# Kernel tuning notes

Measured on AMD Instinct MI355X. Metric: run time of the kernel, lower is better.

## Reference

```python
import jax, jax.numpy as jnp
import numpy as np

SEQ = 4096
EMB = 1024
OUT = 1024


def setup_inputs() -> dict:
    key = jax.random.key(0)
    k_x, k_q, k_k, k_v = jax.random.split(key, 4)
    scale = 1.0 / np.sqrt(EMB)
    inputs = jax.random.normal(k_x, (SEQ, EMB), dtype=jnp.float32)
    # torch Linear weight is (out_features, in_features); y = x @ W.T
    W_Q = jax.random.normal(k_q, (OUT, EMB), dtype=jnp.float32) * scale
    W_K = jax.random.normal(k_k, (OUT, EMB), dtype=jnp.float32) * scale
    W_V = jax.random.normal(k_v, (OUT, EMB), dtype=jnp.float32) * scale
    return {"inputs": inputs, "W_Q": W_Q, "W_K": W_K, "W_V": W_V}


def reference(inputs, W_Q, W_K, W_V):
    # projections: (S, E) @ (E, D) -> (S, D)
    q = inputs @ W_Q.T
    k = inputs @ W_K.T
    v = inputs @ W_V.T
    d_k = k.shape[-1]
    scores = (q @ k.T) / jnp.sqrt(jnp.asarray(d_k, dtype=q.dtype))  # (S, S)
    weights = jax.nn.softmax(scores, axis=-1)
    return weights @ v  # (S, D)
```

## Files before the change

kernel.cpp:

```cpp
#include <hip/hip_runtime.h>

typedef __bf16 bf16;
typedef __bf16 bf16x4 __attribute__((ext_vector_type(4)));
typedef __bf16 bf16x8 __attribute__((ext_vector_type(8)));
typedef float f32x4 __attribute__((ext_vector_type(4)));

#define SEQ 4096
#define EMB 1024

__device__ __forceinline__ void async_copy16(void* lds, const void* g) {
    __builtin_amdgcn_global_load_lds(
        (const __attribute__((address_space(1))) unsigned int*)g,
        (__attribute__((address_space(3))) unsigned int*)lds,
        16, 0, 0);
}

__global__ __launch_bounds__(256) void prep_all(const float* __restrict__ x,
                                                const float* __restrict__ wq,
                                                const float* __restrict__ wk,
                                                const float* __restrict__ wv,
                                                bf16* __restrict__ xb,
                                                bf16* __restrict__ wqk,
                                                bf16* __restrict__ wvb,
                                                float* __restrict__ rowsum)
{
    const int u = blockIdx.x * 256 + threadIdx.x;
    const float* src;
    bf16* dst;
    int off;
    if (u < 1048576)      { src = x;  dst = xb;               off = u; }
    else if (u < 1310720) { src = wq; dst = wqk;              off = u - 1048576; }
    else if (u < 1572864) { src = wk; dst = wqk + EMB * EMB;  off = u - 1310720; }
    else if (u < 1835008) { src = wv; dst = wvb;              off = u - 1572864; }
    else {
        *(float4*)(rowsum + (size_t)(u - 1835008) * 4) = float4{0.f, 0.f, 0.f, 0.f};
        return;
    }
    float4 f = *(const float4*)(src + (size_t)off * 4);
    bf16x4 v = { (bf16)f.x, (bf16)f.y, (bf16)f.z, (bf16)f.w };
    *(bf16x4*)(dst + (size_t)off * 4) = v;
}

template<bool RSUM>
__device__ __forceinline__ void tile_step(int t, int NT,
                                          const bf16* __restrict__ Ab,
                                          const bf16* __restrict__ Bb,
                                          int lda, int ldb,
                                          bf16* __restrict__ As,
                                          bf16* __restrict__ Bs,
                                          bf16* __restrict__ AsD,
                                          bf16* __restrict__ BsD,
                                          int wr, int wc, int fr, int pc,
                                          bf16x8 (&afA)[4], bf16x8 (&afB)[4],
                                          bf16x8 (&bgC)[4], bf16x8 (&bgN)[4],
                                          f32x4 (&acc)[8][4], float (&rsum)[8],
                                          bool rs_active)
{
    if (t + 3 < NT) {
        const int b3 = ((t + 3) & 3) * 8192;
        async_copy16(AsD + b3,        Ab + (t + 3) * 32);
        async_copy16(AsD + b3 + 4096, Ab + (t + 3) * 32 + (size_t)128 * lda);
    }
    {
        const bf16* At = As + (t & 3) * 8192 + (wr * 128 + 64 + fr) * 32 + pc;
#pragma unroll
        for (int mf = 0; mf < 4; mf++)
            afB[mf] = *(const bf16x8*)(At + (mf * 16) * 32);
    }
    asm volatile("s_waitcnt lgkmcnt(4)" ::: "memory");
    __builtin_amdgcn_sched_barrier(0);
    __builtin_amdgcn_s_setprio(1);
#pragma unroll
    for (int nj = 0; nj < 4; nj++)
#pragma unroll
        for (int mf = 0; mf < 4; mf++)
            acc[mf][nj] = __builtin_amdgcn_mfma_f32_16x16x32_bf16(afA[mf], bgC[nj], acc[mf][nj], 0, 0, 0);
    __builtin_amdgcn_s_setprio(0);
    if (RSUM && rs_active) {
#pragma unroll
        for (int mf = 0; mf < 4; mf++)
#pragma unroll
            for (int e = 0; e < 8; e++) rsum[mf] += (float)afA[mf][e];
    }

    if (t < NT - 1) {
        if (t + 3 < NT) {
            asm volatile("s_waitcnt vmcnt(6)" ::: "memory");
        } else if (t + 2 < NT) {
            asm volatile("s_waitcnt vmcnt(4)" ::: "memory");
        } else {
            asm volatile("s_waitcnt vmcnt(0)" ::: "memory");
        }
        __builtin_amdgcn_s_barrier();
        if (t + 3 < NT) {
            const int b3 = ((t + 3) & 3) * 8192;
            async_copy16(BsD + b3,        Bb + (t + 3) * 32);
            async_copy16(BsD + b3 + 4096, Bb + (t + 3) * 32 + (size_t)128 * ldb);
        }
        {
            const int b1 = ((t + 1) & 3) * 8192;
            const bf16* At = As + b1 + (wr * 128 + fr) * 32 + pc;
            const bf16* Bt = Bs + b1 + (wc * 64 + fr) * 32 + pc;
#pragma unroll
            for (int mf = 0; mf < 4; mf++)
                afA[mf] = *(const bf16x8*)(At + (mf * 16) * 32);
#pragma unroll
            for (int nj = 0; nj < 4; nj++)
                bgN[nj] = *(const bf16x8*)(Bt + (nj * 16) * 32);
        }
        asm volatile("s_waitcnt lgkmcnt(8)" ::: "memory");
        __builtin_amdgcn_sched_barrier(0);
    } else {
        asm volatile("s_waitcnt lgkmcnt(0)" ::: "memory");
        __builtin_amdgcn_sched_barrier(0);
    }
    __builtin_amdgcn_s_setprio(1);
#pragma unroll
    for (int nj = 0; nj < 4; nj++)
#pragma unroll
        for (int mf = 0; mf < 4; mf++)
            acc[4 + mf][nj] = __builtin_amdgcn_mfma_f32_16x16x32_bf16(afB[mf], bgC[nj], acc[4 + mf][nj], 0, 0, 0);
    __builtin_amdgcn_s_setprio(0);
    if (RSUM && rs_active) {
#pragma unroll
        for (int mf = 0; mf < 4; mf++)
#pragma unroll
            for (int e = 0; e < 8; e++) rsum[4 + mf] += (float)afB[mf][e];
    }
}

template<bool RSUM>
__device__ __forceinline__ void gemm_core256(const bf16* __restrict__ A,
                                             const bf16* __restrict__ B,
                                             int lda, int ldb, long koff,
                                             int m0, int n0,
                                             bf16* __restrict__ As,
                                             bf16* __restrict__ Bs,
                                             f32x4 (&acc)[8][4], float (&rsum)[8],
                                             bool rs_active)
{
    const int tid  = threadIdx.x;
    const int lane = tid & 63;
    const int wave = tid >> 6;
    const int wr = wave >> 2;
    const int wc = wave & 3;
    const int srow = tid >> 2;
    const int spc  = tid & 3;
    const int sl   = (spc - ((srow >> 1) & 3)) & 3;
    const int fr = lane & 15;
    const int q  = lane >> 4;
    const int pc = ((q + ((fr >> 1) & 3)) & 3) * 8;
    const int NT = 32;

#pragma unroll
    for (int i = 0; i < 8; i++)
#pragma unroll
        for (int j = 0; j < 4; j++) acc[i][j] = {0.f, 0.f, 0.f, 0.f};
    if (RSUM)
#pragma unroll
        for (int i = 0; i < 8; i++) rsum[i] = 0.f;

    const bf16* Ab = A + (size_t)(m0 + srow) * lda + koff + sl * 8;
    const bf16* Bb = B + (size_t)(n0 + srow) * ldb + koff + sl * 8;
    bf16* AsD = As + srow * 32 + spc * 8;
    bf16* BsD = Bs + srow * 32 + spc * 8;

#pragma unroll
    for (int tt = 0; tt < 3; tt++) {
        async_copy16(AsD + tt * 8192,        Ab + tt * 32);
        async_copy16(AsD + tt * 8192 + 4096, Ab + tt * 32 + (size_t)128 * lda);
        async_copy16(BsD + tt * 8192,        Bb + tt * 32);
        async_copy16(BsD + tt * 8192 + 4096, Bb + tt * 32 + (size_t)128 * ldb);
    }
    asm volatile("s_waitcnt vmcnt(8)" ::: "memory");
    __builtin_amdgcn_s_barrier();

    bf16x8 afA[4], afB[4], bg0[4], bg1[4];
    {
        const bf16* At = As + (wr * 128 + fr) * 32 + pc;
        const bf16* Bt = Bs + (wc * 64 + fr) * 32 + pc;
#pragma unroll
        for (int mf = 0; mf < 4; mf++)
            afA[mf] = *(const bf16x8*)(At + (mf * 16) * 32);
#pragma unroll
        for (int nj = 0; nj < 4; nj++)
            bg0[nj] = *(const bf16x8*)(Bt + (nj * 16) * 32);
    }

    for (int t = 0; t < NT; t += 2) {
        tile_step<RSUM>(t,     NT, Ab, Bb, lda, ldb, As, Bs, AsD, BsD,
                        wr, wc, fr, pc, afA, afB, bg0, bg1, acc, rsum, rs_active);
        tile_step<RSUM>(t + 1, NT, Ab, Bb, lda, ldb, As, Bs, AsD, BsD,
                        wr, wc, fr, pc, afA, afB, bg1, bg0, acc, rsum, rs_active);
    }
}

__global__ __launch_bounds__(512, 1) void gemm_proj(const bf16* __restrict__ xb,
                                                    const bf16* __restrict__ wqk,
                                                    const bf16* __restrict__ wvb,
                                                    bf16* __restrict__ QK,
                                                    bf16* __restrict__ VT)
{
    __shared__ __align__(16) bf16 As[4][8192];
    __shared__ __align__(16) bf16 Bs[4][8192];

    const int hw  = blockIdx.x + 16 * blockIdx.y;
    const int xcd = hw & 7;
    const int s   = hw >> 3;
    const int bx  = ((xcd & 1) << 3) | (s & 7);
    const int byy = (xcd >> 1) * 3 + (s >> 3);

    const bf16 *A, *B;
    bf16* C;
    int ldc, m0, n0;
    if (byy < 8) {
        A = xb; B = wqk; C = QK; ldc = 2048;
        m0 = bx * 256; n0 = byy * 256;
    } else {
        const int id = bx + (byy - 8) * 16;
        A = wvb; B = xb; C = VT; ldc = 4096;
        m0 = (id & 3) * 256; n0 = (id >> 2) * 256;
    }

    f32x4 acc[8][4];
    float rs[8];
    gemm_core256<false>(A, B, 1024, 1024, 0, m0, n0, &As[0][0], &Bs[0][0], acc, rs, false);

    const int lane = threadIdx.x & 63;
    const int wave = threadIdx.x >> 6;
    const int cm = m0 + (wave >> 2) * 128 + ((lane >> 4) << 2);
    const int cn = n0 + (wave & 3) * 64 + (lane & 15);
#pragma unroll
    for (int i = 0; i < 8; i++)
#pragma unroll
        for (int j = 0; j < 4; j++)
#pragma unroll
            for (int r = 0; r < 4; r++)
                C[(size_t)(cm + i * 16 + r) * ldc + (cn + j * 16)] = (bf16)acc[i][j][r];
}

__global__ __launch_bounds__(512, 1) void gemm_exp(const bf16* __restrict__ QK,
                                                   bf16* __restrict__ E)
{
    __shared__ __align__(16) bf16 As[4][8192];
    __shared__ __align__(16) bf16 Bs[4][8192];

    const int hw  = blockIdx.x + 16 * blockIdx.y;
    const int xcd = hw & 7;
    const int s   = hw >> 3;
    const int bx  = ((xcd & 1) << 3) | (s & 7);
    const int by  = ((xcd >> 1) << 2) | (s >> 3);

    const int m0 = bx * 256;
    const int n0 = by * 256;
    f32x4 acc[8][4];
    float rs[8];
    gemm_core256<false>(QK, QK + 1024, 2048, 2048, 0, m0, n0, &As[0][0], &Bs[0][0], acc, rs, false);

    const int lane = threadIdx.x & 63;
    const int wave = threadIdx.x >> 6;
    const int cm = m0 + (wave >> 2) * 128 + ((lane >> 4) << 2);
    const int cn = n0 + (wave & 3) * 64 + (lane & 15);
#pragma unroll
    for (int i = 0; i < 8; i++)
#pragma unroll
        for (int j = 0; j < 4; j++)
#pragma unroll
            for (int r = 0; r < 4; r++)
                E[(size_t)(cm + i * 16 + r) * 4096 + (cn + j * 16)] =
                    (bf16)__expf(acc[i][j][r] * 0.03125f);
}

__global__ __launch_bounds__(512, 1) void gemm_pv(const bf16* __restrict__ E,
                                                  const bf16* __restrict__ VT,
                                                  float* __restrict__ out,
                                                  float* __restrict__ p1,
                                                  float* __restrict__ rowsum)
{
    __shared__ __align__(16) bf16 As[4][8192];
    __shared__ __align__(16) bf16 Bs[4][8192];

    const int hw  = blockIdx.x + 16 * blockIdx.y + 64 * blockIdx.z;
    const int xcd = hw & 7;
    const int s   = hw >> 3;
    const int bx  = ((xcd & 1) << 3) | (s & 7);
    const int by  = s >> 3;
    const int bz  = xcd >> 1;

    const int m0 = bx * 256;
    const int n0 = by * 256;
    const long koff = (long)bz * 1024;
    const bool rs_active = (by == 0) && (((threadIdx.x >> 6) & 3) == 0);

    f32x4 acc[8][4];
    float rs[8];
    gemm_core256<true>(E, VT, 4096, 4096, koff, m0, n0, &As[0][0], &Bs[0][0], acc, rs, rs_active);

    const int lane = threadIdx.x & 63;
    const int wave = threadIdx.x >> 6;
    if (rs_active) {
#pragma unroll
        for (int i = 0; i < 8; i++) {
            rs[i] += __shfl_xor(rs[i], 16);
            rs[i] += __shfl_xor(rs[i], 32);
        }
        if (lane < 16) {
            const int rbase = m0 + (wave >> 2) * 128;
#pragma unroll
            for (int i = 0; i < 8; i++)
                unsafeAtomicAdd(&rowsum[rbase + i * 16 + lane], rs[i]);
        }
    }

    float* C = (bz == 0) ? out : p1 + (size_t)(bz - 1) * SEQ * 1024;
    const int cm = m0 + (wave >> 2) * 128 + ((lane >> 4) << 2);
    const int cn = n0 + (wave & 3) * 64 + (lane & 15);
#pragma unroll
    for (int i = 0; i < 8; i++)
#pragma unroll
        for (int j = 0; j < 4; j++)
#pragma unroll
            for (int r = 0; r < 4; r++)
                C[(size_t)(cm + i * 16 + r) * 1024 + (cn + j * 16)] = acc[i][j][r];
}

__global__ __launch_bounds__(256) void reduce_norm(float* __restrict__ out,
                                                   const float* __restrict__ p1,
                                                   const float* __restrict__ p2,
                                                   const float* __restrict__ p3,
                                                   const float* __restrict__ rowsum)
{
    const int m = blockIdx.x;
    const float inv = 1.f / rowsum[m];
    const size_t off = (size_t)m * 1024 + threadIdx.x * 4;
    float4 a = *(const float4*)(out + off);
    float4 b = *(const float4*)(p1 + off);
    float4 c = *(const float4*)(p2 + off);
    float4 d = *(const float4*)(p3 + off);
    float4 o;
    o.x = (a.x + b.x + c.x + d.x) * inv;
    o.y = (a.y + b.y + c.y + d.y) * inv;
    o.z = (a.z + b.z + c.z + d.z) * inv;
    o.w = (a.w + b.w + c.w + d.w) * inv;
    *(float4*)(out + off) = o;
}

extern "C" void kernel_launch(void* const* d_in, const int* in_sizes, int n_in,
                              void* d_out, int out_size, void* d_ws, size_t ws_size,
                              hipStream_t stream)
{
    const float* x  = (const float*)d_in[0];
    const float* wq = (const float*)d_in[1];
    const float* wk = (const float*)d_in[2];
    const float* wv = (const float*)d_in[3];
    float* out = (float*)d_out;

    char* ws = (char*)d_ws;
    const size_t MB = 1024 * 1024;
    bf16*  E   = (bf16*)(ws);
    float* p1  = (float*)(ws + 32 * MB);
    float* p2  = (float*)(ws + 48 * MB);
    float* p3  = (float*)(ws + 64 * MB);
    bf16*  xb  = (bf16*)(ws + 32 * MB);
    bf16*  wqk = (bf16*)(ws + 40 * MB);
    bf16*  wvb = (bf16*)(ws + 44 * MB);
    bf16*  QK  = (bf16*)(ws + 64 * MB);
    bf16*  VT  = (bf16*)(ws + 80 * MB);
    float* rsm = (float*)(ws + 88 * MB);

    prep_all<<<dim3(7172), dim3(256), 0, stream>>>(x, wq, wk, wv, xb, wqk, wvb, rsm);
    gemm_proj<<<dim3(16, 12), dim3(512), 0, stream>>>(xb, wqk, wvb, QK, VT);
    gemm_exp<<<dim3(16, 16), dim3(512), 0, stream>>>(QK, E);
    gemm_pv<<<dim3(16, 4, 4), dim3(512), 0, stream>>>(E, VT, out, p1, rsm);
    reduce_norm<<<dim3(4096), dim3(256), 0, stream>>>(out, p1, p2, p3, rsm);
}
```

Measured before the change: 200.5 us.

## Fuse all attention stages into one persistent cooperative kernel with grid syncs

Replaces the five separate launches (convert, projection GEMM, QK^T+exp GEMM, PV GEMM, reduce/normalize) with a single cooperative kernel of 256 blocks. Stages are separated by grid.sync and thread fences, and the elementwise phases become grid-stride loops. This is meant to remove inter-kernel launch gaps and tail drain between stages. In exchange it adds grid-wide barrier cost, and it requires all 256 blocks of 512 threads to be co-resident.

```diff
diff --git a/kernel.cpp b/kernel.cpp
--- a/kernel.cpp
+++ b/kernel.cpp
@@ -1,4 +1,7 @@
 #include <hip/hip_runtime.h>
+#include <hip/hip_cooperative_groups.h>
+
+namespace cg = cooperative_groups;
 
 typedef __bf16 bf16;
 typedef __bf16 bf16x4 __attribute__((ext_vector_type(4)));
@@ -13,32 +16,6 @@
         (const __attribute__((address_space(1))) unsigned int*)g,
         (__attribute__((address_space(3))) unsigned int*)lds,
         16, 0, 0);
-}
-
-__global__ __launch_bounds__(256) void prep_all(const float* __restrict__ x,
-                                                const float* __restrict__ wq,
-                                                const float* __restrict__ wk,
-                                                const float* __restrict__ wv,
-                                                bf16* __restrict__ xb,
-                                                bf16* __restrict__ wqk,
-                                                bf16* __restrict__ wvb,
-                                                float* __restrict__ rowsum)
-{
-    const int u = blockIdx.x * 256 + threadIdx.x;
-    const float* src;
-    bf16* dst;
-    int off;
-    if (u < 1048576)      { src = x;  dst = xb;               off = u; }
-    else if (u < 1310720) { src = wq; dst = wqk;              off = u - 1048576; }
-    else if (u < 1572864) { src = wk; dst = wqk + EMB * EMB;  off = u - 1310720; }
-    else if (u < 1835008) { src = wv; dst = wvb;              off = u - 1572864; }
-    else {
-        *(float4*)(rowsum + (size_t)(u - 1835008) * 4) = float4{0.f, 0.f, 0.f, 0.f};
-        return;
-    }
-    float4 f = *(const float4*)(src + (size_t)off * 4);
-    bf16x4 v = { (bf16)f.x, (bf16)f.y, (bf16)f.z, (bf16)f.w };
-    *(bf16x4*)(dst + (size_t)off * 4) = v;
 }
 
 template<bool RSUM>
@@ -195,154 +172,162 @@
     }
 }
 
-__global__ __launch_bounds__(512, 1) void gemm_proj(const bf16* __restrict__ xb,
-                                                    const bf16* __restrict__ wqk,
-                                                    const bf16* __restrict__ wvb,
-                                                    bf16* __restrict__ QK,
-                                                    bf16* __restrict__ VT)
+__global__ __launch_bounds__(512, 1) void fused_attn(
+    const float* __restrict__ x,  const float* __restrict__ wq,
+    const float* __restrict__ wk, const float* __restrict__ wv,
+    bf16* __restrict__ xb,  bf16* __restrict__ wqk, bf16* __restrict__ wvb,
+    bf16* __restrict__ QK,  bf16* __restrict__ VT,  bf16* __restrict__ E,
+    float* __restrict__ p1, float* __restrict__ p2, float* __restrict__ p3,
+    float* __restrict__ rowsum, float* __restrict__ out)
 {
     __shared__ __align__(16) bf16 As[4][8192];
     __shared__ __align__(16) bf16 Bs[4][8192];
 
-    const int hw  = blockIdx.x + 16 * blockIdx.y;
-    const int xcd = hw & 7;
-    const int s   = hw >> 3;
-    const int bx  = ((xcd & 1) << 3) | (s & 7);
-    const int byy = (xcd >> 1) * 3 + (s >> 3);
-
-    const bf16 *A, *B;
-    bf16* C;
-    int ldc, m0, n0;
-    if (byy < 8) {
-        A = xb; B = wqk; C = QK; ldc = 2048;
-        m0 = bx * 256; n0 = byy * 256;
-    } else {
-        const int id = bx + (byy - 8) * 16;
-        A = wvb; B = xb; C = VT; ldc = 4096;
-        m0 = (id & 3) * 256; n0 = (id >> 2) * 256;
-    }
+    cg::grid_group grid = cg::this_grid();
+    const int bid  = blockIdx.x;
+    const int tid  = threadIdx.x;
+    const int lane = tid & 63;
+    const int wave = tid >> 6;
+
+    for (int u = bid * 512 + tid; u < 1836032; u += 131072) {
+        const float* src; bf16* dst; int off;
+        if (u < 1048576)      { src = x;  dst = xb;               off = u; }
+        else if (u < 1310720) { src = wq; dst = wqk;              off = u - 1048576; }
+        else if (u < 1572864) { src = wk; dst = wqk + EMB * EMB;  off = u - 1310720; }
+        else if (u < 1835008) { src = wv; dst = wvb;              off = u - 1572864; }
+        else {
+            *(float4*)(rowsum + (size_t)(u - 1835008) * 4) = float4{0.f, 0.f, 0.f, 0.f};
+            continue;
+        }
+        float4 f = *(const float4*)(src + (size_t)off * 4);
+        bf16x4 v = { (bf16)f.x, (bf16)f.y, (bf16)f.z, (bf16)f.w };
+        *(bf16x4*)(dst + (size_t)off * 4) = v;
+    }
+    __threadfence();
+    grid.sync();
+    __threadfence();
 
     f32x4 acc[8][4];
     float rs[8];
-    gemm_core256<false>(A, B, 1024, 1024, 0, m0, n0, &As[0][0], &Bs[0][0], acc, rs, false);
-
-    const int lane = threadIdx.x & 63;
-    const int wave = threadIdx.x >> 6;
-    const int cm = m0 + (wave >> 2) * 128 + ((lane >> 4) << 2);
-    const int cn = n0 + (wave & 3) * 64 + (lane & 15);
-#pragma unroll
-    for (int i = 0; i < 8; i++)
-#pragma unroll
-        for (int j = 0; j < 4; j++)
-#pragma unroll
-            for (int r = 0; r < 4; r++)
-                C[(size_t)(cm + i * 16 + r) * ldc + (cn + j * 16)] = (bf16)acc[i][j][r];
-}
-
-__global__ __launch_bounds__(512, 1) void gemm_exp(const bf16* __restrict__ QK,
-                                                   bf16* __restrict__ E)
-{
-    __shared__ __align__(16) bf16 As[4][8192];
-    __shared__ __align__(16) bf16 Bs[4][8192];
-
-    const int hw  = blockIdx.x + 16 * blockIdx.y;
-    const int xcd = hw & 7;
-    const int s   = hw >> 3;
-    const int bx  = ((xcd & 1) << 3) | (s & 7);
-    const int by  = ((xcd >> 1) << 2) | (s >> 3);
-
-    const int m0 = bx * 256;
-    const int n0 = by * 256;
-    f32x4 acc[8][4];
-    float rs[8];
-    gemm_core256<false>(QK, QK + 1024, 2048, 2048, 0, m0, n0, &As[0][0], &Bs[0][0], acc, rs, false);
-
-    const int lane = threadIdx.x & 63;
-    const int wave = threadIdx.x >> 6;
-    const int cm = m0 + (wave >> 2) * 128 + ((lane >> 4) << 2);
-    const int cn = n0 + (wave & 3) * 64 + (lane & 15);
-#pragma unroll
-    for (int i = 0; i < 8; i++)
-#pragma unroll
-        for (int j = 0; j < 4; j++)
-#pragma unroll
-            for (int r = 0; r < 4; r++)
-                E[(size_t)(cm + i * 16 + r) * 4096 + (cn + j * 16)] =
-                    (bf16)__expf(acc[i][j][r] * 0.03125f);
-}
-
-__global__ __launch_bounds__(512, 1) void gemm_pv(const bf16* __restrict__ E,
-                                                  const bf16* __restrict__ VT,
-                                                  float* __restrict__ out,
-                                                  float* __restrict__ p1,
-                                                  float* __restrict__ rowsum)
-{
-    __shared__ __align__(16) bf16 As[4][8192];
-    __shared__ __align__(16) bf16 Bs[4][8192];
-
-    const int hw  = blockIdx.x + 16 * blockIdx.y + 64 * blockIdx.z;
-    const int xcd = hw & 7;
-    const int s   = hw >> 3;
-    const int bx  = ((xcd & 1) << 3) | (s & 7);
-    const int by  = s >> 3;
-    const int bz  = xcd >> 1;
-
-    const int m0 = bx * 256;
-    const int n0 = by * 256;
-    const long koff = (long)bz * 1024;
-    const bool rs_active = (by == 0) && (((threadIdx.x >> 6) & 3) == 0);
-
-    f32x4 acc[8][4];
-    float rs[8];
-    gemm_core256<true>(E, VT, 4096, 4096, koff, m0, n0, &As[0][0], &Bs[0][0], acc, rs, rs_active);
-
-    const int lane = threadIdx.x & 63;
-    const int wave = threadIdx.x >> 6;
-    if (rs_active) {
-#pragma unroll
-        for (int i = 0; i < 8; i++) {
-            rs[i] += __shfl_xor(rs[i], 16);
-            rs[i] += __shfl_xor(rs[i], 32);
-        }
-        if (lane < 16) {
-            const int rbase = m0 + (wave >> 2) * 128;
-#pragma unroll
-            for (int i = 0; i < 8; i++)
-                unsafeAtomicAdd(&rowsum[rbase + i * 16 + lane], rs[i]);
-        }
-    }
-
-    float* C = (bz == 0) ? out : p1 + (size_t)(bz - 1) * SEQ * 1024;
-    const int cm = m0 + (wave >> 2) * 128 + ((lane >> 4) << 2);
-    const int cn = n0 + (wave & 3) * 64 + (lane & 15);
-#pragma unroll
-    for (int i = 0; i < 8; i++)
-#pragma unroll
-        for (int j = 0; j < 4; j++)
-#pragma unroll
-            for (int r = 0; r < 4; r++)
-                C[(size_t)(cm + i * 16 + r) * 1024 + (cn + j * 16)] = acc[i][j][r];
-}
-
-__global__ __launch_bounds__(256) void reduce_norm(float* __restrict__ out,
-                                                   const float* __restrict__ p1,
-                                                   const float* __restrict__ p2,
-                                                   const float* __restrict__ p3,
-                                                   const float* __restrict__ rowsum)
-{
-    const int m = blockIdx.x;
-    const float inv = 1.f / rowsum[m];
-    const size_t off = (size_t)m * 1024 + threadIdx.x * 4;
-    float4 a = *(const float4*)(out + off);
-    float4 b = *(const float4*)(p1 + off);
-    float4 c = *(const float4*)(p2 + off);
-    float4 d = *(const float4*)(p3 + off);
-    float4 o;
-    o.x = (a.x + b.x + c.x + d.x) * inv;
-    o.y = (a.y + b.y + c.y + d.y) * inv;
-    o.z = (a.z + b.z + c.z + d.z) * inv;
-    o.w = (a.w + b.w + c.w + d.w) * inv;
-    *(float4*)(out + off) = o;
+
+    if (bid < 192) {
+        const int xcd = bid & 7;
+        const int s   = bid >> 3;
+        const int bx  = ((xcd & 1) << 3) | (s & 7);
+        const int byy = (xcd >> 1) * 3 + (s >> 3);
+
+        const bf16 *A, *B;
+        bf16* C;
+        int ldc, m0, n0;
+        if (byy < 8) {
+            A = xb; B = wqk; C = QK; ldc = 2048;
+            m0 = bx * 256; n0 = byy * 256;
+        } else {
+            const int id = bx + (byy - 8) * 16;
+            A = wvb; B = xb; C = VT; ldc = 4096;
+            m0 = (id & 3) * 256; n0 = (id >> 2) * 256;
+        }
+
+        gemm_core256<false>(A, B, 1024, 1024, 0, m0, n0, &As[0][0], &Bs[0][0], acc, rs, false);
+
+        const int cm = m0 + (wave >> 2) * 128 + ((lane >> 4) << 2);
+        const int cn = n0 + (wave & 3) * 64 + (lane & 15);
+#pragma unroll
+        for (int i = 0; i < 8; i++)
+#pragma unroll
+            for (int j = 0; j < 4; j++)
+#pragma unroll
+                for (int r = 0; r < 4; r++)
+                    C[(size_t)(cm + i * 16 + r) * ldc + (cn + j * 16)] = (bf16)acc[i][j][r];
+    }
+    __threadfence();
+    grid.sync();
+    __threadfence();
+
+    {
+        const int xcd = bid & 7;
+        const int s   = bid >> 3;
+        const int bx  = ((xcd & 1) << 3) | (s & 7);
+        const int by  = ((xcd >> 1) << 2) | (s >> 3);
+        const int m0 = bx * 256;
+        const int n0 = by * 256;
+
+        gemm_core256<false>(QK, QK + 1024, 2048, 2048, 0, m0, n0, &As[0][0], &Bs[0][0], acc, rs, false);
+
+        const int cm = m0 + (wave >> 2) * 128 + ((lane >> 4) << 2);
+        const int cn = n0 + (wave & 3) * 64 + (lane & 15);
+#pragma unroll
+        for (int i = 0; i < 8; i++)
+#pragma unroll
+            for (int j = 0; j < 4; j++)
+#pragma unroll
+                for (int r = 0; r < 4; r++)
+                    E[(size_t)(cm + i * 16 + r) * 4096 + (cn + j * 16)] =
+                        (bf16)__expf(acc[i][j][r] * 0.03125f);
+    }
+    __threadfence();
+    grid.sync();
+    __threadfence();
+
+    {
+        const int xcd = bid & 7;
+        const int s   = bid >> 3;
+        const int bx  = ((xcd & 1) << 3) | (s & 7);
+        const int by  = s >> 3;
+        const int bz  = xcd >> 1;
+        const int m0 = bx * 256;
+        const int n0 = by * 256;
+        const long koff = (long)bz * 1024;
+        const bool rs_active = (by == 0) && (((tid >> 6) & 3) == 0);
+
+        gemm_core256<true>(E, VT, 4096, 4096, koff, m0, n0, &As[0][0], &Bs[0][0], acc, rs, rs_active);
+
+        if (rs_active) {
+#pragma unroll
+            for (int i = 0; i < 8; i++) {
+                rs[i] += __shfl_xor(rs[i], 16);
+                rs[i] += __shfl_xor(rs[i], 32);
+            }
+            if (lane < 16) {
+                const int rbase = m0 + (wave >> 2) * 128;
+#pragma unroll
+                for (int i = 0; i < 8; i++)
+                    unsafeAtomicAdd(&rowsum[rbase + i * 16 + lane], rs[i]);
+            }
+        }
+
+        float* C = (bz == 0) ? out
+                 : (bz == 1) ? p1
+                 : (bz == 2) ? p2 : p3;
+        const int cm = m0 + (wave >> 2) * 128 + ((lane >> 4) << 2);
+        const int cn = n0 + (wave & 3) * 64 + (lane & 15);
+#pragma unroll
+        for (int i = 0; i < 8; i++)
+#pragma unroll
+            for (int j = 0; j < 4; j++)
+#pragma unroll
+                for (int r = 0; r < 4; r++)
+                    C[(size_t)(cm + i * 16 + r) * 1024 + (cn + j * 16)] = acc[i][j][r];
+    }
+    __threadfence();
+    grid.sync();
+    __threadfence();
+
+    for (int u = bid * 512 + tid; u < 1048576; u += 131072) {
+        const int m = u >> 8;
+        const size_t off = (size_t)u * 4;
+        const float inv = 1.f / rowsum[m];
+        float4 a = *(const float4*)(out + off);
+        float4 b = *(const float4*)(p1 + off);
+        float4 c = *(const float4*)(p2 + off);
+        float4 d = *(const float4*)(p3 + off);
+        float4 o;
+        o.x = (a.x + b.x + c.x + d.x) * inv;
+        o.y = (a.y + b.y + c.y + d.y) * inv;
+        o.z = (a.z + b.z + c.z + d.z) * inv;
+        o.w = (a.w + b.w + c.w + d.w) * inv;
+        *(float4*)(out + off) = o;
+    }
 }
 
 extern "C" void kernel_launch(void* const* d_in, const int* in_sizes, int n_in,
@@ -368,9 +353,11 @@
     bf16*  VT  = (bf16*)(ws + 80 * MB);
     float* rsm = (float*)(ws + 88 * MB);
 
-    prep_all<<<dim3(7172), dim3(256), 0, stream>>>(x, wq, wk, wv, xb, wqk, wvb, rsm);
-    gemm_proj<<<dim3(16, 12), dim3(512), 0, stream>>>(xb, wqk, wvb, QK, VT);
-    gemm_exp<<<dim3(16, 16), dim3(512), 0, stream>>>(QK, E);
-    gemm_pv<<<dim3(16, 4, 4), dim3(512), 0, stream>>>(E, VT, out, p1, rsm);
-    reduce_norm<<<dim3(4096), dim3(256), 0, stream>>>(out, p1, p2, p3, rsm);
-}
+    void* args[] = { (void*)&x, (void*)&wq, (void*)&wk, (void*)&wv,
+                     (void*)&xb, (void*)&wqk, (void*)&wvb,
+                     (void*)&QK, (void*)&VT, (void*)&E,
+                     (void*)&p1, (void*)&p2, (void*)&p3,
+                     (void*)&rsm, (void*)&out };
+    hipLaunchCooperativeKernel((const void*)fused_attn, dim3(256), dim3(512),
+                               args, 0, stream);
+}
```

Result: slower. 716.2 us (+257.1%).
